# Kernel tuning notes

Hardware: AMD Instinct MI355X
Metric: run time of the kernel (lower is better)

Reference implementation:

```python
import jax, jax.numpy as jnp
import numpy as np

N_EMBD = 1568  # 2 * 784, hard-coded in the source module
HEAD_SIZE = 128
BATCH = 16384


def setup_inputs() -> dict:
    key = jax.random.key(0)
    kx, kq, kk, kv = jax.random.split(key, 4)
    x = jax.random.normal(kx, (BATCH, N_EMBD), dtype=jnp.float32)
    wq = jax.random.normal(kq, (N_EMBD, HEAD_SIZE), dtype=jnp.float32) * (N_EMBD ** -0.5)
    wk = jax.random.normal(kk, (N_EMBD, HEAD_SIZE), dtype=jnp.float32) * (N_EMBD ** -0.5)
    wv = jax.random.normal(kv, (N_EMBD, HEAD_SIZE), dtype=jnp.float32) * (N_EMBD ** -0.5)
    return {"x": x, "wq": wq, "wk": wk, "wv": wv}


def reference(x, wq, wk, wv):
    # x: [B, N]; projections (bias-free Linear): [B, H]
    B, N = x.shape
    q = x @ wq
    k = x @ wk
    v = x @ wv
    # Outer-product score matrix per batch element: [B, H, H]
    attn = jnp.einsum('bi,bj->bij', q, k) * (N ** -0.5)  # scale uses FEATURE dim N, as in source
    attn = jax.nn.softmax(attn, axis=-1)
    # dropout is identity in eval mode
    out = jnp.einsum('bij,bj->bi', attn, v)  # [B, H]
    return out
```

## Files before the change

kernel.cpp:

```cpp
#include <hip/hip_runtime.h>
#include <stdint.h>

typedef unsigned short u16;
typedef __bf16 bf16x8 __attribute__((ext_vector_type(8)));
typedef float f32x4 __attribute__((ext_vector_type(4)));

#define M_ROWS 16384
#define K_DIM  1568
#define H_DIM  128
#define MT     32
#define BK     32
#define K0LEN  768
#define K1LEN  800
#define ASTR   808
#define PSTR   132
#define SCALE  0.02525381361380526f
#define LOG2E  1.4426950408889634f

__device__ __forceinline__ u16 f32_to_bf16_rne(float f) {
    uint32_t u = __float_as_uint(f);
    uint32_t r = (u + 0x7FFFu + ((u >> 16) & 1u)) >> 16;
    return (u16)r;
}

#define MFMA(a, b, c) __builtin_amdgcn_mfma_f32_16x16x32_bf16(a, b, c, 0, 0, 0)

__global__ __launch_bounds__(256) void wtrans_kernel(
    const float* __restrict__ wq, const float* __restrict__ wk,
    const float* __restrict__ wv, u16* __restrict__ wt)
{
    __shared__ u16 tile[32][33];
    const float* w = (blockIdx.z == 0) ? wq : (blockIdx.z == 1) ? wk : wv;
    const int k0 = blockIdx.x * 32;
    const int n0 = blockIdx.y * 32;

    const int tn = threadIdx.x & 31;
    const int tk = threadIdx.x >> 5;
    #pragma unroll
    for (int p = 0; p < 4; p++) {
        int kk = tk + p * 8;
        tile[kk][tn] = f32_to_bf16_rne(w[(size_t)(k0 + kk) * H_DIM + n0 + tn]);
    }
    __syncthreads();

    u16* dst = wt + (size_t)blockIdx.z * H_DIM * K_DIM;
    const int tk2 = threadIdx.x & 31;
    const int tn2 = threadIdx.x >> 5;
    #pragma unroll
    for (int p = 0; p < 4; p++) {
        int nn = tn2 + p * 8;
        dst[(size_t)(n0 + nn) * K_DIM + k0 + tk2] = tile[tk2][nn];
    }
}

__global__ __launch_bounds__(512, 4) void fused_kernel(
    const float* __restrict__ x,
    const u16* __restrict__ wt,
    float* __restrict__ out)
{
    __shared__ char smem[MT * ASTR * 2];
    u16*  Abuf = (u16*)smem;
    float (*Pq)[PSTR] = (float (*)[PSTR])smem;
    float (*Pk)[PSTR] = (float (*)[PSTR])(smem + MT * PSTR * 4);
    float (*Pv)[PSTR] = (float (*)[PSTR])(smem + 2 * MT * PSTR * 4);

    const int tid  = threadIdx.x;
    const int lane = tid & 63;
    const int wave = tid >> 6;
    const int lrow = lane & 15;
    const int quad = lane >> 4;
    const int m0   = blockIdx.x * MT;

    const u16* bp[3];
    #pragma unroll
    for (int nt = 0; nt < 3; nt++) {
        int ng = wave * 48 + nt * 16 + lrow;
        bp[nt] = wt + (size_t)(ng >> 7) * (H_DIM * K_DIM)
                    + (size_t)(ng & 127) * K_DIM + quad * 8;
    }

    const int srow = tid >> 4;
    const int st16 = tid & 15;
    const float* xrow = x + (size_t)(m0 + srow) * K_DIM;

    f32x4 acc[2][3] = {};
    const u16* a_ld0 = &Abuf[(0 * 16 + lrow) * ASTR + quad * 8];
    const u16* a_ld1 = &Abuf[(1 * 16 + lrow) * ASTR + quad * 8];

    for (int i = st16; i < K0LEN / 4; i += 16) {
        float4 f = *(const float4*)(xrow + i * 4);
        union { u16 h[4]; uint2 v; } p;
        p.h[0] = f32_to_bf16_rne(f.x); p.h[1] = f32_to_bf16_rne(f.y);
        p.h[2] = f32_to_bf16_rne(f.z); p.h[3] = f32_to_bf16_rne(f.w);
        *(uint2*)&Abuf[srow * ASTR + i * 4] = p.v;
    }
    __syncthreads();

    bf16x8 b0 = *(const bf16x8*)(bp[0]);
    bf16x8 b1 = *(const bf16x8*)(bp[1]);
    bf16x8 b2 = *(const bf16x8*)(bp[2]);

    #pragma unroll 2
    for (int it = 0; it < 24; it++) {
        const int kn = (it + 1) * BK;
        bf16x8 bn0 = *(const bf16x8*)(bp[0] + kn);
        bf16x8 bn1 = *(const bf16x8*)(bp[1] + kn);
        bf16x8 bn2 = *(const bf16x8*)(bp[2] + kn);

        bf16x8 a0 = *(const bf16x8*)(a_ld0 + it * BK);
        bf16x8 a1 = *(const bf16x8*)(a_ld1 + it * BK);

        acc[0][0] = MFMA(a0, b0, acc[0][0]);
        acc[1][0] = MFMA(a1, b0, acc[1][0]);
        acc[0][1] = MFMA(a0, b1, acc[0][1]);
        acc[1][1] = MFMA(a1, b1, acc[1][1]);
        acc[0][2] = MFMA(a0, b2, acc[0][2]);
        acc[1][2] = MFMA(a1, b2, acc[1][2]);

        b0 = bn0; b1 = bn1; b2 = bn2;
    }
    __syncthreads();

    for (int i = st16; i < K1LEN / 4; i += 16) {
        float4 f = *(const float4*)(xrow + K0LEN + i * 4);
        union { u16 h[4]; uint2 v; } p;
        p.h[0] = f32_to_bf16_rne(f.x); p.h[1] = f32_to_bf16_rne(f.y);
        p.h[2] = f32_to_bf16_rne(f.z); p.h[3] = f32_to_bf16_rne(f.w);
        *(uint2*)&Abuf[srow * ASTR + i * 4] = p.v;
    }
    __syncthreads();

    #pragma unroll 2
    for (int it = 0; it < 25; it++) {
        int kn = K0LEN + (it + 1) * BK;
        if (kn > K_DIM - BK) kn = K_DIM - BK;
        bf16x8 bn0 = *(const bf16x8*)(bp[0] + kn);
        bf16x8 bn1 = *(const bf16x8*)(bp[1] + kn);
        bf16x8 bn2 = *(const bf16x8*)(bp[2] + kn);

        bf16x8 a0 = *(const bf16x8*)(a_ld0 + it * BK);
        bf16x8 a1 = *(const bf16x8*)(a_ld1 + it * BK);

        acc[0][0] = MFMA(a0, b0, acc[0][0]);
        acc[1][0] = MFMA(a1, b0, acc[1][0]);
        acc[0][1] = MFMA(a0, b1, acc[0][1]);
        acc[1][1] = MFMA(a1, b1, acc[1][1]);
        acc[0][2] = MFMA(a0, b2, acc[0][2]);
        acc[1][2] = MFMA(a1, b2, acc[1][2]);

        b0 = bn0; b1 = bn1; b2 = bn2;
    }
    __syncthreads();

    #pragma unroll
    for (int mt = 0; mt < 2; mt++) {
        #pragma unroll
        for (int nt = 0; nt < 3; nt++) {
            const int base = wave * 48 + nt * 16;
            const int sel  = base >> 7;
            const int col  = (base & 127) + lrow;
            const int mrow = mt * 16 + quad * 4;
            if (sel == 0) {
                #pragma unroll
                for (int r = 0; r < 4; r++)
                    Pq[mrow + r][col] = acc[mt][nt][r] * (SCALE * LOG2E);
            } else if (sel == 1) {
                #pragma unroll
                for (int r = 0; r < 4; r++)
                    Pk[mrow + r][col] = acc[mt][nt][r];
            } else {
                #pragma unroll
                for (int r = 0; r < 4; r++)
                    Pv[mrow + r][col] = acc[mt][nt][r];
            }
        }
    }
    __syncthreads();

    const int r   = tid >> 4;
    const int sub = tid & 15;

    float qq[8], num[8], den[8];
    #pragma unroll
    for (int ii = 0; ii < 8; ii++) {
        qq[ii]  = Pq[r][sub * 8 + ii];
        num[ii] = 0.f;
        den[ii] = 0.f;
    }

    #pragma unroll 4
    for (int j = 0; j < 128; j++) {
        float kj = Pk[r][j];
        float vj = Pv[r][j];
        #pragma unroll
        for (int ii = 0; ii < 8; ii++) {
            float e = __builtin_amdgcn_exp2f(qq[ii] * kj);
            den[ii] += e;
            num[ii] += e * vj;
        }
    }

    float* op = out + (size_t)(m0 + r) * H_DIM + sub * 8;
    #pragma unroll
    for (int g = 0; g < 2; g++) {
        float4 o;
        o.x = num[4 * g + 0] / den[4 * g + 0];
        o.y = num[4 * g + 1] / den[4 * g + 1];
        o.z = num[4 * g + 2] / den[4 * g + 2];
        o.w = num[4 * g + 3] / den[4 * g + 3];
        *(float4*)(op + 4 * g) = o;
    }
}

extern "C" void kernel_launch(void* const* d_in, const int* in_sizes, int n_in,
                              void* d_out, int out_size, void* d_ws, size_t ws_size,
                              hipStream_t stream)
{
    const float* x  = (const float*)d_in[0];
    const float* wq = (const float*)d_in[1];
    const float* wk = (const float*)d_in[2];
    const float* wv = (const float*)d_in[3];
    float* out = (float*)d_out;

    u16* wt = (u16*)d_ws;

    wtrans_kernel<<<dim3(K_DIM / 32, H_DIM / 32, 3), 256, 0, stream>>>(wq, wk, wv, wt);
    fused_kernel<<<M_ROWS / MT, 512, 0, stream>>>(x, wt, out);
}
```

Before: 222.5 us.

## Block weight layout by K-step, deepen B prefetch, use nontemporal x/out access

The transposed weights are stored in K-step-major blocks ([49][384][32]), so each wave's B fragment loads for one K step come from a contiguous region instead of rows strided by K_DIM. B prefetch goes from one to two steps ahead, and the first B loads are issued before the barrier. Loads of x and stores of out become nontemporal to keep the streamed activations from evicting the weights in cache, and the min-blocks hint is dropped from launch bounds. The deeper prefetch uses more registers, which may lower occupancy.

Result: faster. 212.3 us (-4.6%).

```diff
diff --git a/kernel.cpp b/kernel.cpp
--- a/kernel.cpp
+++ b/kernel.cpp
@@ -8,12 +8,15 @@
 #define M_ROWS 16384
 #define K_DIM  1568
 #define H_DIM  128
+#define NQ     384
 #define MT     32
 #define BK     32
+#define NSTEP  49
 #define K0LEN  768
 #define K1LEN  800
 #define ASTR   808
 #define PSTR   132
+#define KSTRIDE (NQ * BK)
 #define SCALE  0.02525381361380526f
 #define LOG2E  1.4426950408889634f
 
@@ -27,35 +30,36 @@
 
 __global__ __launch_bounds__(256) void wtrans_kernel(
     const float* __restrict__ wq, const float* __restrict__ wk,
-    const float* __restrict__ wv, u16* __restrict__ wt)
+    const float* __restrict__ wv, u16* __restrict__ wt2)
 {
     __shared__ u16 tile[32][33];
     const float* w = (blockIdx.z == 0) ? wq : (blockIdx.z == 1) ? wk : wv;
     const int k0 = blockIdx.x * 32;
-    const int n0 = blockIdx.y * 32;
+    const int nloc0 = blockIdx.y * 32;
+    const int ng0 = blockIdx.z * 128 + nloc0;
 
     const int tn = threadIdx.x & 31;
     const int tk = threadIdx.x >> 5;
     #pragma unroll
     for (int p = 0; p < 4; p++) {
         int kk = tk + p * 8;
-        tile[kk][tn] = f32_to_bf16_rne(w[(size_t)(k0 + kk) * H_DIM + n0 + tn]);
-    }
-    __syncthreads();
-
-    u16* dst = wt + (size_t)blockIdx.z * H_DIM * K_DIM;
-    const int tk2 = threadIdx.x & 31;
+        tile[kk][tn] = f32_to_bf16_rne(w[(size_t)(k0 + kk) * H_DIM + nloc0 + tn]);
+    }
+    __syncthreads();
+
+    const int klo = threadIdx.x & 31;
     const int tn2 = threadIdx.x >> 5;
+    u16* dst = wt2 + (size_t)(k0 >> 5) * KSTRIDE;
     #pragma unroll
     for (int p = 0; p < 4; p++) {
         int nn = tn2 + p * 8;
-        dst[(size_t)(n0 + nn) * K_DIM + k0 + tk2] = tile[tk2][nn];
-    }
-}
-
-__global__ __launch_bounds__(512, 4) void fused_kernel(
+        dst[(size_t)(ng0 + nn) * 32 + klo] = tile[klo][nn];
+    }
+}
+
+__global__ __launch_bounds__(512) void fused_kernel(
     const float* __restrict__ x,
-    const u16* __restrict__ wt,
+    const u16* __restrict__ wt2,
     float* __restrict__ out)
 {
     __shared__ char smem[MT * ASTR * 2];
@@ -75,8 +79,7 @@
     #pragma unroll
     for (int nt = 0; nt < 3; nt++) {
         int ng = wave * 48 + nt * 16 + lrow;
-        bp[nt] = wt + (size_t)(ng >> 7) * (H_DIM * K_DIM)
-                    + (size_t)(ng & 127) * K_DIM + quad * 8;
+        bp[nt] = wt2 + (size_t)ng * 32 + quad * 8;
     }
 
     const int srow = tid >> 4;
@@ -88,41 +91,45 @@
     const u16* a_ld1 = &Abuf[(1 * 16 + lrow) * ASTR + quad * 8];
 
     for (int i = st16; i < K0LEN / 4; i += 16) {
-        float4 f = *(const float4*)(xrow + i * 4);
+        f32x4 f = __builtin_nontemporal_load((const f32x4*)(xrow + i * 4));
         union { u16 h[4]; uint2 v; } p;
         p.h[0] = f32_to_bf16_rne(f.x); p.h[1] = f32_to_bf16_rne(f.y);
         p.h[2] = f32_to_bf16_rne(f.z); p.h[3] = f32_to_bf16_rne(f.w);
         *(uint2*)&Abuf[srow * ASTR + i * 4] = p.v;
     }
-    __syncthreads();
-
-    bf16x8 b0 = *(const bf16x8*)(bp[0]);
-    bf16x8 b1 = *(const bf16x8*)(bp[1]);
-    bf16x8 b2 = *(const bf16x8*)(bp[2]);
+
+    bf16x8 B0[3], B1[3];
+    #pragma unroll
+    for (int nt = 0; nt < 3; nt++) {
+        B0[nt] = *(const bf16x8*)(bp[nt]);
+        B1[nt] = *(const bf16x8*)(bp[nt] + KSTRIDE);
+    }
+    __syncthreads();
 
     #pragma unroll 2
     for (int it = 0; it < 24; it++) {
-        const int kn = (it + 1) * BK;
-        bf16x8 bn0 = *(const bf16x8*)(bp[0] + kn);
-        bf16x8 bn1 = *(const bf16x8*)(bp[1] + kn);
-        bf16x8 bn2 = *(const bf16x8*)(bp[2] + kn);
+        const size_t kpf = (size_t)(it + 2) * KSTRIDE;
+        bf16x8 B2_0 = *(const bf16x8*)(bp[0] + kpf);
+        bf16x8 B2_1 = *(const bf16x8*)(bp[1] + kpf);
+        bf16x8 B2_2 = *(const bf16x8*)(bp[2] + kpf);
 
         bf16x8 a0 = *(const bf16x8*)(a_ld0 + it * BK);
         bf16x8 a1 = *(const bf16x8*)(a_ld1 + it * BK);
 
-        acc[0][0] = MFMA(a0, b0, acc[0][0]);
-        acc[1][0] = MFMA(a1, b0, acc[1][0]);
-        acc[0][1] = MFMA(a0, b1, acc[0][1]);
-        acc[1][1] = MFMA(a1, b1, acc[1][1]);
-        acc[0][2] = MFMA(a0, b2, acc[0][2]);
-        acc[1][2] = MFMA(a1, b2, acc[1][2]);
-
-        b0 = bn0; b1 = bn1; b2 = bn2;
+        acc[0][0] = MFMA(a0, B0[0], acc[0][0]);
+        acc[1][0] = MFMA(a1, B0[0], acc[1][0]);
+        acc[0][1] = MFMA(a0, B0[1], acc[0][1]);
+        acc[1][1] = MFMA(a1, B0[1], acc[1][1]);
+        acc[0][2] = MFMA(a0, B0[2], acc[0][2]);
+        acc[1][2] = MFMA(a1, B0[2], acc[1][2]);
+
+        B0[0] = B1[0]; B0[1] = B1[1]; B0[2] = B1[2];
+        B1[0] = B2_0;  B1[1] = B2_1;  B1[2] = B2_2;
     }
     __syncthreads();
 
     for (int i = st16; i < K1LEN / 4; i += 16) {
-        float4 f = *(const float4*)(xrow + K0LEN + i * 4);
+        f32x4 f = __builtin_nontemporal_load((const f32x4*)(xrow + K0LEN + i * 4));
         union { u16 h[4]; uint2 v; } p;
         p.h[0] = f32_to_bf16_rne(f.x); p.h[1] = f32_to_bf16_rne(f.y);
         p.h[2] = f32_to_bf16_rne(f.z); p.h[3] = f32_to_bf16_rne(f.w);
@@ -132,23 +139,25 @@
 
     #pragma unroll 2
     for (int it = 0; it < 25; it++) {
-        int kn = K0LEN + (it + 1) * BK;
-        if (kn > K_DIM - BK) kn = K_DIM - BK;
-        bf16x8 bn0 = *(const bf16x8*)(bp[0] + kn);
-        bf16x8 bn1 = *(const bf16x8*)(bp[1] + kn);
-        bf16x8 bn2 = *(const bf16x8*)(bp[2] + kn);
+        int kg = 24 + it + 2;
+        if (kg > NSTEP - 1) kg = NSTEP - 1;
+        const size_t kpf = (size_t)kg * KSTRIDE;
+        bf16x8 B2_0 = *(const bf16x8*)(bp[0] + kpf);
+        bf16x8 B2_1 = *(const bf16x8*)(bp[1] + kpf);
+        bf16x8 B2_2 = *(const bf16x8*)(bp[2] + kpf);
 
         bf16x8 a0 = *(const bf16x8*)(a_ld0 + it * BK);
         bf16x8 a1 = *(const bf16x8*)(a_ld1 + it * BK);
 
-        acc[0][0] = MFMA(a0, b0, acc[0][0]);
-        acc[1][0] = MFMA(a1, b0, acc[1][0]);
-        acc[0][1] = MFMA(a0, b1, acc[0][1]);
-        acc[1][1] = MFMA(a1, b1, acc[1][1]);
-        acc[0][2] = MFMA(a0, b2, acc[0][2]);
-        acc[1][2] = MFMA(a1, b2, acc[1][2]);
-
-        b0 = bn0; b1 = bn1; b2 = bn2;
+        acc[0][0] = MFMA(a0, B0[0], acc[0][0]);
+        acc[1][0] = MFMA(a1, B0[0], acc[1][0]);
+        acc[0][1] = MFMA(a0, B0[1], acc[0][1]);
+        acc[1][1] = MFMA(a1, B0[1], acc[1][1]);
+        acc[0][2] = MFMA(a0, B0[2], acc[0][2]);
+        acc[1][2] = MFMA(a1, B0[2], acc[1][2]);
+
+        B0[0] = B1[0]; B0[1] = B1[1]; B0[2] = B1[2];
+        B1[0] = B2_0;  B1[1] = B2_1;  B1[2] = B2_2;
     }
     __syncthreads();
 
@@ -203,12 +212,12 @@
     float* op = out + (size_t)(m0 + r) * H_DIM + sub * 8;
     #pragma unroll
     for (int g = 0; g < 2; g++) {
-        float4 o;
+        f32x4 o;
         o.x = num[4 * g + 0] / den[4 * g + 0];
         o.y = num[4 * g + 1] / den[4 * g + 1];
         o.z = num[4 * g + 2] / den[4 * g + 2];
         o.w = num[4 * g + 3] / den[4 * g + 3];
-        *(float4*)(op + 4 * g) = o;
+        __builtin_nontemporal_store(o, (f32x4*)(op + 4 * g));
     }
 }
 
@@ -222,8 +231,8 @@
     const float* wv = (const float*)d_in[3];
     float* out = (float*)d_out;
 
-    u16* wt = (u16*)d_ws;
-
-    wtrans_kernel<<<dim3(K_DIM / 32, H_DIM / 32, 3), 256, 0, stream>>>(wq, wk, wv, wt);
-    fused_kernel<<<M_ROWS / MT, 512, 0, stream>>>(x, wt, out);
-}
+    u16* wt2 = (u16*)d_ws;
+
+    wtrans_kernel<<<dim3(K_DIM / 32, H_DIM / 32, 3), 256, 0, stream>>>(wq, wk, wv, wt2);
+    fused_kernel<<<M_ROWS / MT, 512, 0, stream>>>(x, wt2, out);
+}
```
